# Kernel optimization log

Hardware: AMD Instinct MI355X
Metric: run time of the kernel (lower is better)

Reference implementation:

```python
import jax, jax.numpy as jnp
import numpy as np

B, S, D, H = 8, 1024, 512, 8
Dh = D // H
MASK_FILL = -1e32


def _xavier_uniform(key, shape):
    fan_in, fan_out = shape[-1], shape[-2] if len(shape) > 1 else shape[-1]
    limit = float(np.sqrt(6.0 / (fan_in + fan_out)))
    return jax.random.uniform(key, shape, jnp.float32, -limit, limit)


def setup_inputs() -> dict:
    key = jax.random.key(0)
    ks = jax.random.split(key, 8)
    q = jax.random.normal(ks[0], (B, S, D), jnp.float32)
    k = jax.random.normal(ks[1], (B, S, D), jnp.float32)
    v = jax.random.normal(ks[2], (B, S, D), jnp.float32)
    # causal mask, broadcast over batch and heads
    mask = jnp.tril(jnp.ones((S, S), dtype=bool))[None, None]
    # key_query_same=True -> one shared W for q and k
    Wq = _xavier_uniform(ks[3], (D, D)); bq = jnp.zeros((D,), jnp.float32)
    Wv = _xavier_uniform(ks[4], (D, D)); bv = jnp.zeros((D,), jnp.float32)
    Wo = _xavier_uniform(ks[5], (D, D)); bo = jnp.zeros((D,), jnp.float32)
    # gammas: (H,1,1), xavier_uniform with fan_in=fan_out=1 -> limit sqrt(3)
    lim = float(np.sqrt(3.0))
    gammas = jax.random.uniform(ks[6], (H, 1, 1), jnp.float32, -lim, lim)
    return {"q": q, "k": k, "v": v, "mask": mask,
            "Wq": Wq, "bq": bq, "Wv": Wv, "bv": bv,
            "Wo": Wo, "bo": bo, "gammas": gammas}


def reference(q, k, v, mask, Wq, bq, Wv, bv, Wo, bo, gammas):
    b, s, d = q.shape
    # projections (key_query_same -> Wq used for both q and k)
    qh = (jnp.einsum("bsd,ed->bse", q, Wq) + bq).reshape(b, s, H, Dh).transpose(0, 2, 1, 3)
    kh = (jnp.einsum("bsd,ed->bse", k, Wq) + bq).reshape(b, s, H, Dh).transpose(0, 2, 1, 3)
    vh = (jnp.einsum("bsd,ed->bse", v, Wv) + bv).reshape(b, s, H, Dh).transpose(0, 2, 1, 3)

    scale = 1.0 / jnp.sqrt(jnp.asarray(Dh, jnp.float32))
    scores = jnp.einsum("bhqd,bhkd->bhqk", qh, kh) * scale  # [B,H,S,S]

    # --- distance-decay effect (no-grad in original) ---
    pos = jnp.arange(s, dtype=jnp.float32)
    position_effect = jnp.abs(pos[None, :] - pos[:, None])[None, None]  # [1,1,S,S]
    scores_ = jax.nn.softmax(jnp.where(mask, scores, MASK_FILL), axis=-1)
    distcum = jnp.cumsum(scores_, axis=-1)
    disttotal = jnp.sum(scores_, axis=-1, keepdims=True)
    dist_scores = jnp.sqrt(jnp.clip((disttotal - distcum) * position_effect, 0.0, None))
    dist_scores = jax.lax.stop_gradient(dist_scores)

    gamma = -jnp.abs(gammas)[None]  # [1,H,1,1]
    total_effect = jnp.clip(jnp.exp(dist_scores * gamma), 1e-5, 1e5)
    scores = scores * total_effect

    scores = jax.nn.softmax(jnp.where(mask, scores, MASK_FILL), axis=-1)
    scores = jnp.where(mask, scores, 0.0)  # hard zero, avoid leakage

    v_ = jnp.einsum("bhqk,bhkd->bhqd", scores, vh)
    concat = v_.transpose(0, 2, 1, 3).reshape(b, s, d)
    output = jnp.einsum("bsd,ed->bse", concat, Wo) + bo
    return output, scores
```

## Files before the change

kernel.cpp:

```cpp
#include <hip/hip_runtime.h>
#include <hip/hip_bf16.h>

#define PB 8
#define PS 1024
#define PD 512
#define PH 8

typedef __attribute__((ext_vector_type(8))) short short8;
typedef __attribute__((ext_vector_type(4))) float f32x4;

__device__ inline ushort f2bf(float x) {
    union { float f; unsigned u; } c; c.f = x;
    unsigned u = c.u + 0x7fffu + ((c.u >> 16) & 1u);
    return (ushort)(u >> 16);
}
__device__ inline float bf2f(ushort u) {
    union { unsigned u; float f; } c; c.u = (unsigned)u << 16; return c.f;
}

__device__ inline void gload16(const void* g, void* l) {
    __builtin_amdgcn_global_load_lds(
        (const __attribute__((address_space(1))) void*)g,
        (__attribute__((address_space(3))) void*)l, 16, 0, 0);
}

__global__ __launch_bounds__(256)
void cast_all(const float* __restrict__ q, const float* __restrict__ k,
              const float* __restrict__ v, const float* __restrict__ Wq,
              const float* __restrict__ Wv, const float* __restrict__ Wo,
              ushort* __restrict__ q_bf, ushort* __restrict__ k_bf,
              ushort* __restrict__ v_bf, ushort* __restrict__ Wq_bf,
              ushort* __restrict__ Wv_bf, ushort* __restrict__ Wo_bf)
{
    const int bid = blockIdx.x;
    const float* s; ushort* d; int base;
    if      (bid < 4096)  { s = q;  d = q_bf;  base = bid; }
    else if (bid < 8192)  { s = k;  d = k_bf;  base = bid - 4096; }
    else if (bid < 12288) { s = v;  d = v_bf;  base = bid - 8192; }
    else if (bid < 12544) { s = Wq; d = Wq_bf; base = bid - 12288; }
    else if (bid < 12800) { s = Wv; d = Wv_bf; base = bid - 12544; }
    else                  { s = Wo; d = Wo_bf; base = bid - 12800; }
    const int i = base * 256 + threadIdx.x;
    const float4 x = ((const float4*)s)[i];
    ushort4 o;
    o.x = f2bf(x.x); o.y = f2bf(x.y); o.z = f2bf(x.z); o.w = f2bf(x.w);
    ((ushort4*)d)[i] = o;
}

__global__ __launch_bounds__(256)
void proj3(const ushort* __restrict__ q_bf, const ushort* __restrict__ k_bf,
           const ushort* __restrict__ v_bf, const ushort* __restrict__ Wq_bf,
           const ushort* __restrict__ Wv_bf, const float* __restrict__ bq,
           const float* __restrict__ bv, ushort* __restrict__ qh,
           ushort* __restrict__ kh, ushort* __restrict__ vhT)
{
    const int z = blockIdx.z;
    const ushort* A = (z == 0) ? q_bf : (z == 1) ? k_bf : v_bf;
    const ushort* B = (z == 2) ? Wv_bf : Wq_bf;
    const float* bias = (z == 2) ? bv : bq;

    __shared__ __align__(16) ushort S[128 * 136];
    ushort* As = S;
    ushort* Bs = S + 8192;
    const int tid = threadIdx.x;
    const int lane = tid & 63;
    const int wave = tid >> 6;
    const int wr = wave >> 1, wc = wave & 1;
    const int bm = blockIdx.x * 128, bn = blockIdx.y * 128;
    const int lrow = lane >> 3;
    const int lcol = (lane & 7) * 8;

    f32x4 acc[4][4] = {};

    for (int k0 = 0; k0 < 512; k0 += 64) {
#pragma unroll
        for (int i = 0; i < 4; ++i) {
            const int c = wave * 4 + i;
            gload16(A + (size_t)(bm + c * 8 + lrow) * 512 + k0 + lcol, &As[c * 512]);
            gload16(B + (size_t)(bn + c * 8 + lrow) * 512 + k0 + lcol, &Bs[c * 512]);
        }
        __syncthreads();
        short8 af[2][4], bf[2][4];
#pragma unroll
        for (int kk = 0; kk < 2; ++kk) {
#pragma unroll
            for (int m = 0; m < 4; ++m)
                af[kk][m] = *(const short8*)&As[(wr * 64 + m * 16 + (lane & 15)) * 64 + kk * 32 + (lane >> 4) * 8];
#pragma unroll
            for (int n = 0; n < 4; ++n)
                bf[kk][n] = *(const short8*)&Bs[(wc * 64 + n * 16 + (lane & 15)) * 64 + kk * 32 + (lane >> 4) * 8];
        }
#pragma unroll
        for (int kk = 0; kk < 2; ++kk)
#pragma unroll
            for (int m = 0; m < 4; ++m)
#pragma unroll
                for (int n = 0; n < 4; ++n)
                    acc[m][n] = __builtin_amdgcn_mfma_f32_16x16x32_bf16(af[kk][m], bf[kk][n], acc[m][n], 0, 0, 0);
        __syncthreads();
    }

    if (z == 2) {
#pragma unroll
        for (int m = 0; m < 4; ++m)
#pragma unroll
            for (int n = 0; n < 4; ++n) {
                const int r0 = wr * 64 + m * 16 + (lane >> 4) * 4;
                const int cl = wc * 64 + n * 16 + (lane & 15);
                const float bi = bias[bn + cl];
                ushort4 o;
                o.x = f2bf(acc[m][n][0] + bi);
                o.y = f2bf(acc[m][n][1] + bi);
                o.z = f2bf(acc[m][n][2] + bi);
                o.w = f2bf(acc[m][n][3] + bi);
                *(ushort4*)&S[cl * 136 + r0] = o;
            }
    } else {
#pragma unroll
        for (int m = 0; m < 4; ++m)
#pragma unroll
            for (int n = 0; n < 4; ++n) {
                const int r0 = wr * 64 + m * 16 + (lane >> 4) * 4;
                const int cl = wc * 64 + n * 16 + (lane & 15);
                const float bi = bias[bn + cl];
#pragma unroll
                for (int r = 0; r < 4; ++r)
                    S[(r0 + r) * 136 + cl] = f2bf(acc[m][n][r] + bi);
            }
    }
    __syncthreads();

    const int b = bm >> 10, sbase = bm & 1023;
    if (z == 2) {
#pragma unroll
        for (int it = 0; it < 8; ++it) {
            const int c = it * 256 + tid;
            const int dloc = c >> 4, seg = c & 15;
            const int h = (bn >> 6) + (dloc >> 6), d = dloc & 63;
            const uint4 v4 = *(const uint4*)&S[dloc * 136 + seg * 8];
            *(uint4*)&vhT[((size_t)((b * 8 + h) * 64 + d)) * 1024 + sbase + seg * 8] = v4;
        }
    } else {
        ushort* out = z ? kh : qh;
#pragma unroll
        for (int it = 0; it < 8; ++it) {
            const int c = it * 256 + tid;
            const int row = c >> 4, seg = c & 15;
            const int h = (bn >> 6) + (seg >> 3), d8 = (seg & 7) * 8;
            const uint4 v4 = *(const uint4*)&S[row * 136 + seg * 8];
            *(uint4*)&out[(((size_t)(b * 8 + h)) * 1024 + sbase + row) * 64 + d8] = v4;
        }
    }
}

__global__ __launch_bounds__(256)
void qk_mfma(const ushort* __restrict__ qh, const ushort* __restrict__ kh,
             float* __restrict__ scores)
{
    const int d0 = blockIdx.x;
    const int bh = d0 & 63;
    const int pair = d0 >> 6;
    const int kb = pair & 7, qb = pair >> 3;
    const int tid = threadIdx.x;
    if (kb > qb) {
        float* S = scores + ((size_t)bh << 20);
        const f32x4 z = {};
#pragma unroll
        for (int it = 0; it < 16; ++it) {
            const int f = it * 256 + tid;
            const int row = f >> 5, c4 = f & 31;
            __builtin_nontemporal_store(z,
                (f32x4*)&S[(size_t)(qb * 128 + row) * 1024 + kb * 128 + c4 * 4]);
        }
        return;
    }
    __shared__ __align__(16) ushort S[128 * 136];
    ushort* As = S;
    ushort* Bs = S + 8192;
    const int lane = tid & 63, wave = tid >> 6;
    const int wr = wave >> 1, wc = wave & 1;
    const ushort* Ab = qh + ((size_t)bh * PS + qb * 128) * 64;
    const ushort* Bb = kh + ((size_t)bh * PS + kb * 128) * 64;

#pragma unroll
    for (int i = 0; i < 4; ++i) {
        const int c = wave * 4 + i;
        gload16(Ab + c * 512 + lane * 8, &As[c * 512]);
        gload16(Bb + c * 512 + lane * 8, &Bs[c * 512]);
    }
    __syncthreads();

    f32x4 acc[4][4] = {};
    short8 af[2][4], bf[2][4];
#pragma unroll
    for (int kk = 0; kk < 2; ++kk) {
#pragma unroll
        for (int m = 0; m < 4; ++m)
            af[kk][m] = *(const short8*)&As[(wr * 64 + m * 16 + (lane & 15)) * 64 + kk * 32 + (lane >> 4) * 8];
#pragma unroll
        for (int n = 0; n < 4; ++n)
            bf[kk][n] = *(const short8*)&Bs[(wc * 64 + n * 16 + (lane & 15)) * 64 + kk * 32 + (lane >> 4) * 8];
    }
#pragma unroll
    for (int kk = 0; kk < 2; ++kk)
#pragma unroll
        for (int m = 0; m < 4; ++m)
#pragma unroll
            for (int n = 0; n < 4; ++n)
                acc[m][n] = __builtin_amdgcn_mfma_f32_16x16x32_bf16(af[kk][m], bf[kk][n], acc[m][n], 0, 0, 0);

    __syncthreads();

#pragma unroll
    for (int m = 0; m < 4; ++m)
#pragma unroll
        for (int n = 0; n < 4; ++n) {
            const int r0 = wr * 64 + m * 16 + (lane >> 4) * 4;
            const int cl = wc * 64 + n * 16 + (lane & 15);
#pragma unroll
            for (int r = 0; r < 4; ++r)
                S[(r0 + r) * 136 + cl] = f2bf(acc[m][n][r] * 0.125f);
        }
    __syncthreads();

    ushort* Sr = (ushort*)(scores + ((size_t)bh << 20));
#pragma unroll
    for (int it = 0; it < 8; ++it) {
        const int c = it * 256 + tid;
        const int row = c >> 4, seg = c & 15;
        const uint4 v4 = *(const uint4*)&S[row * 136 + seg * 8];
        *(uint4*)&Sr[(size_t)(qb * 128 + row) * 2048 + kb * 128 + seg * 8] = v4;
    }
}

__global__ __launch_bounds__(512, 8)
void rowpv3(float* __restrict__ scores, const ushort* __restrict__ vhT,
            const float* __restrict__ gammas, ushort* __restrict__ attn)
{
    const int d0 = blockIdx.x;
    const int bh = d0 & 63, h = bh & 7;
    const int b = bh >> 3;
    const int rb = d0 >> 6;
    const int w = threadIdx.x >> 6;
    const int lane = threadIdx.x & 63;
    const int i = rb * 8 + w;
    const int nt = (rb >> 3) + 1;
    const int G = (nt + 3) >> 2;
    const int base = lane * 4 * G;
    const int lim = ((i >> 7) + 1) * 128;

    __shared__ __align__(16) ushort P[8 * 1024];
    __shared__ float RED[2][8][68];

    float* srow = scores + ((size_t)bh << 20) + ((size_t)i << 10);
    const ushort* rraw = (const ushort*)srow;

    union U4 { uint2 v; ushort u[4]; };
    float l[16];
#pragma unroll
    for (int g = 0; g < 4; ++g) {
        if (g < G) {
            U4 a; a.v = *(const uint2*)(rraw + base + g * 4);
#pragma unroll
            for (int j = 0; j < 4; ++j)
                l[g * 4 + j] = (base + g * 4 + j <= i) ? bf2f(a.u[j]) : -3.0e38f;
        }
    }

    float m1 = -3.0e38f;
#pragma unroll
    for (int g = 0; g < 4; ++g) if (g < G)
#pragma unroll
        for (int j = 0; j < 4; ++j) m1 = fmaxf(m1, l[g * 4 + j]);
#pragma unroll
    for (int off = 32; off; off >>= 1) m1 = fmaxf(m1, __shfl_xor(m1, off));

    float lsum = 0.f;
#pragma unroll
    for (int g = 0; g < 4; ++g) if (g < G)
#pragma unroll
        for (int j = 0; j < 4; ++j) lsum += __expf(l[g * 4 + j] - m1);
    float incl = lsum;
#pragma unroll
    for (int off = 1; off < 64; off <<= 1) {
        const float y = __shfl_up(incl, off);
        if (lane >= off) incl += y;
    }
    const float excl = incl - lsum;
    const float es = __shfl(incl, 63);
    const float inv_es = __builtin_amdgcn_rcpf(es);
    const float gamma = -fabsf(gammas[h]);
    const float M2 = fmaxf(m1, 0.f);

    float racc = excl;
    float s2 = 0.f;
#pragma unroll
    for (int g = 0; g < 4; ++g) if (g < G)
#pragma unroll
        for (int j = 0; j < 4; ++j) {
            const int c = g * 4 + j;
            if (base + c <= i) {
                racc += __expf(l[c] - m1);
                const float sfxn = fmaxf((es - racc) * inv_es, 0.f);
                const float pe = (float)(i - (base + c));
                const float dist = __builtin_amdgcn_sqrtf(sfxn * pe);
                const float eff = fmaxf(__expf(gamma * dist), 1e-5f);
                const float p = __expf(l[c] * eff - M2);
                l[c] = p; s2 += p;
            } else {
                l[c] = 0.f;
            }
        }
#pragma unroll
    for (int off = 32; off; off >>= 1) s2 += __shfl_xor(s2, off);
    const float inv2 = __builtin_amdgcn_rcpf(s2);
#pragma unroll
    for (int g = 0; g < 4; ++g) if (g < G)
#pragma unroll
        for (int j = 0; j < 4; ++j) l[g * 4 + j] *= inv2;

#pragma unroll
    for (int g = 0; g < 4; ++g) {
        if (g < G) {
            U4 p;
#pragma unroll
            for (int j = 0; j < 4; ++j) p.u[j] = f2bf(l[g * 4 + j]);
            const int col = base + g * 4;
            const int lc = col >> 3;
            const int sp = (lc & ~7) | ((lc ^ w) & 7);
            *(uint2*)&P[w * 1024 + sp * 8 + (col & 7)] = p.v;
        }
    }
    __syncthreads();

#pragma unroll
    for (int g = 0; g < 4; ++g) {
        if (g < G && base + g * 4 < lim) {
            f32x4 v;
            v[0] = l[g * 4 + 0]; v[1] = l[g * 4 + 1];
            v[2] = l[g * 4 + 2]; v[3] = l[g * 4 + 3];
            *(f32x4*)&srow[base + g * 4] = v;
        }
    }

    const int kq = w >> 2, nn = w & 3;
    const int row16 = lane & 15, kg = lane >> 4;
    const int arow = lane & 7;
    const ushort* vb = vhT + ((size_t)bh << 16) + (size_t)(nn * 16 + row16) * 1024;
    f32x4 acc = {};
    for (int t = kq; t < nt; t += 2) {
#pragma unroll
        for (int kk = 0; kk < 2; ++kk) {
            const int chunk = t * 8 + ((kk * 4 + kg) ^ arow);
            const short8 af = *(const short8*)&P[arow * 1024 + chunk * 8];
            const short8 bf = *(const short8*)&vb[t * 64 + kk * 32 + kg * 8];
            acc = __builtin_amdgcn_mfma_f32_16x16x32_bf16(af, bf, acc, 0, 0, 0);
        }
    }

    if (kg < 2) {
#pragma unroll
        for (int r = 0; r < 4; ++r)
            RED[kq][kg * 4 + r][nn * 16 + row16] = acc[r];
    }
    __syncthreads();
    const float o = RED[0][w][lane] + RED[1][w][lane];
    attn[((size_t)(b * 1024 + i)) * 512 + h * 64 + lane] = f2bf(o);
}

__global__ __launch_bounds__(256)
void gemm_out(const ushort* __restrict__ A, const ushort* __restrict__ B,
              const float* __restrict__ bias, float* __restrict__ out)
{
    __shared__ __align__(16) ushort As[128 * 64];
    __shared__ __align__(16) ushort Bs[128 * 64];
    const int tid = threadIdx.x;
    const int lane = tid & 63;
    const int wave = tid >> 6;
    const int wr = wave >> 1, wc = wave & 1;
    const int bm = blockIdx.x * 128, bn = blockIdx.y * 128;
    const int lrow = lane >> 3;
    const int lcol = (lane & 7) * 8;

    f32x4 acc[4][4] = {};

    for (int k0 = 0; k0 < 512; k0 += 64) {
#pragma unroll
        for (int i = 0; i < 4; ++i) {
            const int c = wave * 4 + i;
            gload16(A + (size_t)(bm + c * 8 + lrow) * 512 + k0 + lcol, &As[c * 512]);
            gload16(B + (size_t)(bn + c * 8 + lrow) * 512 + k0 + lcol, &Bs[c * 512]);
        }
        __syncthreads();
        short8 af[2][4], bf[2][4];
#pragma unroll
        for (int kk = 0; kk < 2; ++kk) {
#pragma unroll
            for (int m = 0; m < 4; ++m)
                af[kk][m] = *(const short8*)&As[(wr * 64 + m * 16 + (lane & 15)) * 64 + kk * 32 + (lane >> 4) * 8];
#pragma unroll
            for (int n = 0; n < 4; ++n)
                bf[kk][n] = *(const short8*)&Bs[(wc * 64 + n * 16 + (lane & 15)) * 64 + kk * 32 + (lane >> 4) * 8];
        }
#pragma unroll
        for (int kk = 0; kk < 2; ++kk)
#pragma unroll
            for (int m = 0; m < 4; ++m)
#pragma unroll
                for (int n = 0; n < 4; ++n)
                    acc[m][n] = __builtin_amdgcn_mfma_f32_16x16x32_bf16(af[kk][m], bf[kk][n], acc[m][n], 0, 0, 0);
        __syncthreads();
    }

#pragma unroll
    for (int m = 0; m < 4; ++m)
#pragma unroll
        for (int n = 0; n < 4; ++n)
#pragma unroll
            for (int r = 0; r < 4; ++r) {
                const int row = bm + wr * 64 + m * 16 + (lane >> 4) * 4 + r;
                const int col = bn + wc * 64 + n * 16 + (lane & 15);
                out[(size_t)row * 512 + col] = acc[m][n][r] + bias[col];
            }
}

extern "C" void kernel_launch(void* const* d_in, const int* in_sizes, int n_in,
                              void* d_out, int out_size, void* d_ws, size_t ws_size,
                              hipStream_t stream)
{
    const float* q      = (const float*)d_in[0];
    const float* k      = (const float*)d_in[1];
    const float* v      = (const float*)d_in[2];
    const float* Wq     = (const float*)d_in[4];
    const float* bq     = (const float*)d_in[5];
    const float* Wv     = (const float*)d_in[6];
    const float* bv     = (const float*)d_in[7];
    const float* Wo     = (const float*)d_in[8];
    const float* bo     = (const float*)d_in[9];
    const float* gammas = (const float*)d_in[10];

    float* out    = (float*)d_out;
    float* scores = out + (size_t)PB * PS * PD;

    char* w = (char*)d_ws;
    ushort* q_bf  = (ushort*)(w);
    ushort* k_bf  = (ushort*)(w + (8u  << 20));
    ushort* v_bf  = (ushort*)(w + (16u << 20));
    ushort* Wq_bf = (ushort*)(w + (24u << 20));
    ushort* Wv_bf = (ushort*)(w + (24u << 20) + (1u << 19));
    ushort* Wo_bf = (ushort*)(w + (25u << 20));
    ushort* qh    = (ushort*)(w + (26u << 20));
    ushort* kh    = (ushort*)(w + (34u << 20));
    ushort* vhT   = (ushort*)(w + (42u << 20));
    ushort* attn  = (ushort*)(w + (50u << 20));

    cast_all<<<13056, 256, 0, stream>>>(q, k, v, Wq, Wv, Wo,
                                        q_bf, k_bf, v_bf, Wq_bf, Wv_bf, Wo_bf);

    proj3<<<dim3(64, 4, 3), 256, 0, stream>>>(q_bf, k_bf, v_bf, Wq_bf, Wv_bf,
                                              bq, bv, qh, kh, vhT);

    qk_mfma<<<4096, 256, 0, stream>>>(qh, kh, scores);
    rowpv3<<<8192, 512, 0, stream>>>(scores, vhT, gammas, attn);

    gemm_out<<<dim3(64, 4), 256, 0, stream>>>(attn, Wo_bf, bo, out);
}
```

Before: 204.7 us.

## Fuse QK score computation into row softmax/PV kernel via LDS

Removes the separate qk_mfma kernel that wrote bf16 scores into the scores buffer and then reread them. Each rowpv4 block now computes its 8 query rows of QK^T with MFMA directly into shared memory, then runs the existing two-softmax and PV path, and zero-fills the masked tail of each score row itself. This saves a global write and read of the intermediate scores and one kernel launch. In exchange, the K tiles are loaded redundantly by every 8-row block, which means far more K traffic per block than the 128-row tiles did, and launch bounds drop to 4 blocks per SM.

```diff
diff --git a/kernel.cpp b/kernel.cpp
--- a/kernel.cpp
+++ b/kernel.cpp
@@ -153,89 +153,10 @@
     }
 }
 
-__global__ __launch_bounds__(256)
-void qk_mfma(const ushort* __restrict__ qh, const ushort* __restrict__ kh,
-             float* __restrict__ scores)
-{
-    const int d0 = blockIdx.x;
-    const int bh = d0 & 63;
-    const int pair = d0 >> 6;
-    const int kb = pair & 7, qb = pair >> 3;
-    const int tid = threadIdx.x;
-    if (kb > qb) {
-        float* S = scores + ((size_t)bh << 20);
-        const f32x4 z = {};
-#pragma unroll
-        for (int it = 0; it < 16; ++it) {
-            const int f = it * 256 + tid;
-            const int row = f >> 5, c4 = f & 31;
-            __builtin_nontemporal_store(z,
-                (f32x4*)&S[(size_t)(qb * 128 + row) * 1024 + kb * 128 + c4 * 4]);
-        }
-        return;
-    }
-    __shared__ __align__(16) ushort S[128 * 136];
-    ushort* As = S;
-    ushort* Bs = S + 8192;
-    const int lane = tid & 63, wave = tid >> 6;
-    const int wr = wave >> 1, wc = wave & 1;
-    const ushort* Ab = qh + ((size_t)bh * PS + qb * 128) * 64;
-    const ushort* Bb = kh + ((size_t)bh * PS + kb * 128) * 64;
-
-#pragma unroll
-    for (int i = 0; i < 4; ++i) {
-        const int c = wave * 4 + i;
-        gload16(Ab + c * 512 + lane * 8, &As[c * 512]);
-        gload16(Bb + c * 512 + lane * 8, &Bs[c * 512]);
-    }
-    __syncthreads();
-
-    f32x4 acc[4][4] = {};
-    short8 af[2][4], bf[2][4];
-#pragma unroll
-    for (int kk = 0; kk < 2; ++kk) {
-#pragma unroll
-        for (int m = 0; m < 4; ++m)
-            af[kk][m] = *(const short8*)&As[(wr * 64 + m * 16 + (lane & 15)) * 64 + kk * 32 + (lane >> 4) * 8];
-#pragma unroll
-        for (int n = 0; n < 4; ++n)
-            bf[kk][n] = *(const short8*)&Bs[(wc * 64 + n * 16 + (lane & 15)) * 64 + kk * 32 + (lane >> 4) * 8];
-    }
-#pragma unroll
-    for (int kk = 0; kk < 2; ++kk)
-#pragma unroll
-        for (int m = 0; m < 4; ++m)
-#pragma unroll
-            for (int n = 0; n < 4; ++n)
-                acc[m][n] = __builtin_amdgcn_mfma_f32_16x16x32_bf16(af[kk][m], bf[kk][n], acc[m][n], 0, 0, 0);
-
-    __syncthreads();
-
-#pragma unroll
-    for (int m = 0; m < 4; ++m)
-#pragma unroll
-        for (int n = 0; n < 4; ++n) {
-            const int r0 = wr * 64 + m * 16 + (lane >> 4) * 4;
-            const int cl = wc * 64 + n * 16 + (lane & 15);
-#pragma unroll
-            for (int r = 0; r < 4; ++r)
-                S[(r0 + r) * 136 + cl] = f2bf(acc[m][n][r] * 0.125f);
-        }
-    __syncthreads();
-
-    ushort* Sr = (ushort*)(scores + ((size_t)bh << 20));
-#pragma unroll
-    for (int it = 0; it < 8; ++it) {
-        const int c = it * 256 + tid;
-        const int row = c >> 4, seg = c & 15;
-        const uint4 v4 = *(const uint4*)&S[row * 136 + seg * 8];
-        *(uint4*)&Sr[(size_t)(qb * 128 + row) * 2048 + kb * 128 + seg * 8] = v4;
-    }
-}
-
-__global__ __launch_bounds__(512, 8)
-void rowpv3(float* __restrict__ scores, const ushort* __restrict__ vhT,
-            const float* __restrict__ gammas, ushort* __restrict__ attn)
+__global__ __launch_bounds__(512, 4)
+void rowpv4(const ushort* __restrict__ qh, const ushort* __restrict__ kh,
+            const ushort* __restrict__ vhT, const float* __restrict__ gammas,
+            float* __restrict__ scores, ushort* __restrict__ attn)
 {
     const int d0 = blockIdx.x;
     const int bh = d0 & 63, h = bh & 7;
@@ -249,18 +170,45 @@
     const int base = lane * 4 * G;
     const int lim = ((i >> 7) + 1) * 128;
 
-    __shared__ __align__(16) ushort P[8 * 1024];
+    __shared__ __align__(16) ushort SL[8 * 1024];
     __shared__ float RED[2][8][68];
 
+    const int l15 = lane & 15, lg = lane >> 4;
+    const int arow = lane & 7;
+    {
+        short8 aq[2];
+#pragma unroll
+        for (int kk = 0; kk < 2; ++kk)
+            aq[kk] = *(const short8*)&qh[((size_t)bh * 1024 + rb * 8 + arow) * 64 + kk * 32 + lg * 8];
+        for (int t = w; t < nt; t += 8) {
+            f32x4 qacc[4] = {};
+#pragma unroll
+            for (int kk = 0; kk < 2; ++kk)
+#pragma unroll
+                for (int n = 0; n < 4; ++n) {
+                    const short8 bk = *(const short8*)&kh[((size_t)bh * 1024 + t * 64 + n * 16 + l15) * 64 + kk * 32 + lg * 8];
+                    qacc[n] = __builtin_amdgcn_mfma_f32_16x16x32_bf16(aq[kk], bk, qacc[n], 0, 0, 0);
+                }
+            if (lg < 2) {
+#pragma unroll
+                for (int n = 0; n < 4; ++n)
+#pragma unroll
+                    for (int r = 0; r < 4; ++r)
+                        SL[(lg * 4 + r) * 1024 + t * 64 + n * 16 + l15] = f2bf(qacc[n][r] * 0.125f);
+            }
+        }
+    }
+    __syncthreads();
+
     float* srow = scores + ((size_t)bh << 20) + ((size_t)i << 10);
-    const ushort* rraw = (const ushort*)srow;
+    const ushort* rl = &SL[w * 1024];
 
     union U4 { uint2 v; ushort u[4]; };
     float l[16];
 #pragma unroll
     for (int g = 0; g < 4; ++g) {
         if (g < G) {
-            U4 a; a.v = *(const uint2*)(rraw + base + g * 4);
+            U4 a; a.v = *(const uint2*)(rl + base + g * 4);
 #pragma unroll
             for (int j = 0; j < 4; ++j)
                 l[g * 4 + j] = (base + g * 4 + j <= i) ? bf2f(a.u[j]) : -3.0e38f;
@@ -328,7 +276,7 @@
             const int col = base + g * 4;
             const int lc = col >> 3;
             const int sp = (lc & ~7) | ((lc ^ w) & 7);
-            *(uint2*)&P[w * 1024 + sp * 8 + (col & 7)] = p.v;
+            *(uint2*)&SL[w * 1024 + sp * 8 + (col & 7)] = p.v;
         }
     }
     __syncthreads();
@@ -342,26 +290,29 @@
             *(f32x4*)&srow[base + g * 4] = v;
         }
     }
+    {
+        const f32x4 z = {};
+        for (int c0 = lim + lane * 4; c0 < 1024; c0 += 256)
+            __builtin_nontemporal_store(z, (f32x4*)&srow[c0]);
+    }
 
     const int kq = w >> 2, nn = w & 3;
-    const int row16 = lane & 15, kg = lane >> 4;
-    const int arow = lane & 7;
-    const ushort* vb = vhT + ((size_t)bh << 16) + (size_t)(nn * 16 + row16) * 1024;
+    const ushort* vb = vhT + ((size_t)bh << 16) + (size_t)(nn * 16 + l15) * 1024;
     f32x4 acc = {};
     for (int t = kq; t < nt; t += 2) {
 #pragma unroll
         for (int kk = 0; kk < 2; ++kk) {
-            const int chunk = t * 8 + ((kk * 4 + kg) ^ arow);
-            const short8 af = *(const short8*)&P[arow * 1024 + chunk * 8];
-            const short8 bf = *(const short8*)&vb[t * 64 + kk * 32 + kg * 8];
+            const int chunk = t * 8 + ((kk * 4 + lg) ^ arow);
+            const short8 af = *(const short8*)&SL[arow * 1024 + chunk * 8];
+            const short8 bf = *(const short8*)&vb[t * 64 + kk * 32 + lg * 8];
             acc = __builtin_amdgcn_mfma_f32_16x16x32_bf16(af, bf, acc, 0, 0, 0);
         }
     }
 
-    if (kg < 2) {
+    if (lg < 2) {
 #pragma unroll
         for (int r = 0; r < 4; ++r)
-            RED[kq][kg * 4 + r][nn * 16 + row16] = acc[r];
+            RED[kq][lg * 4 + r][nn * 16 + l15] = acc[r];
     }
     __syncthreads();
     const float o = RED[0][w][lane] + RED[1][w][lane];
@@ -460,8 +411,7 @@
     proj3<<<dim3(64, 4, 3), 256, 0, stream>>>(q_bf, k_bf, v_bf, Wq_bf, Wv_bf,
                                               bq, bv, qh, kh, vhT);
 
-    qk_mfma<<<4096, 256, 0, stream>>>(qh, kh, scores);
-    rowpv3<<<8192, 512, 0, stream>>>(scores, vhT, gammas, attn);
+    rowpv4<<<8192, 512, 0, stream>>>(qh, kh, vhT, gammas, scores, attn);
 
     gemm_out<<<dim3(64, 4), 256, 0, stream>>>(attn, Wo_bf, bo, out);
 }
```

Measured after the change: 238.4 us. 16.5% more time.
